# Performance work log

Hardware: AMD Instinct MI355X
Metric: run time of the kernel (lower is better)

## Reference

```python
import jax, jax.numpy as jnp
import numpy as np

B, S, E, H = 8, 2048, 512, 4
D = E // H


def setup_inputs() -> dict:
    key = jax.random.key(0)
    ks = jax.random.split(key, 9)
    std = 0.05  # keras 'normal' initializer default stddev
    return {
        "x": jax.random.normal(ks[0], (B, S, E), dtype=jnp.float32),
        "Wq": jax.random.normal(ks[1], (E, E), dtype=jnp.float32) * std,
        "Wk": jax.random.normal(ks[2], (E, E), dtype=jnp.float32) * std,
        "Wv": jax.random.normal(ks[3], (E, E), dtype=jnp.float32) * std,
        "Wepi": jax.random.normal(ks[4], (S, S), dtype=jnp.float32) * std,
        "bq": jax.random.normal(ks[5], (S, 1), dtype=jnp.float32) * std,
        "bk": jax.random.normal(ks[6], (S, 1), dtype=jnp.float32) * std,
        "bv": jax.random.normal(ks[7], (S, 1), dtype=jnp.float32) * std,
        "bo": jax.random.normal(ks[8], (S, 1), dtype=jnp.float32) * std,
    }


def reference(x, Wq, Wk, Wv, Wepi, bq, bk, bv, bo):
    b, s, e = x.shape
    # QKV projections; [S,1] biases broadcast across the feature dim
    q = x @ Wq + bq  # [B,S,E]
    k = x @ Wk + bk
    v = x @ Wv + bv
    # split heads -> [B,H,S,D]
    q = q.reshape(b, s, H, D).transpose(0, 2, 1, 3)
    k = k.reshape(b, s, H, D).transpose(0, 2, 1, 3)
    v = v.reshape(b, s, H, D).transpose(0, 2, 1, 3)
    # NOTE: source scales by sqrt(seq_length), not sqrt(head_dim)
    scale = 1.0 / np.sqrt(float(s)).astype(np.float32)
    scores = jnp.einsum("bhsd,bhtd->bhst", q, k) * scale  # [B,H,S,S]
    attn = jax.nn.softmax(scores, axis=-1)
    # epigenomic multiplicative mask applied AFTER softmax (broadcast [S,S])
    attn = attn * Wepi
    effect = jnp.einsum("bhst,bhtd->bhsd", attn, v)  # [B,H,S,D]
    effect = effect.transpose(0, 2, 1, 3).reshape(b, s, e) + bo
    # original returns attention in merged-batch layout [B*H, S, S]
    return effect, attn.reshape(b * H, s, s)
```

## Files before the change

### kernel.cpp

```cpp
#include <hip/hip_runtime.h>
#include <hip/hip_bf16.h>

constexpr int Bn = 8, Sn = 2048, En = 512, Hn = 4, Dn = 128;
constexpr int BHn = Bn * Hn;
constexpr int Mqkv = Bn * Sn;

typedef __attribute__((ext_vector_type(8))) short short8;
typedef __attribute__((ext_vector_type(4))) float f32x4;

__device__ __forceinline__ unsigned short f2bf(float f) {
  unsigned int u = __builtin_bit_cast(unsigned int, f);
  u += 0x7FFF + ((u >> 16) & 1);
  return (unsigned short)(u >> 16);
}

__device__ __forceinline__ void bar_pub() {
  asm volatile("s_waitcnt lgkmcnt(0)" ::: "memory");
  __builtin_amdgcn_s_barrier();
  asm volatile("" ::: "memory");
}

__global__ __launch_bounds__(256) void qkv_kernel(
    const float* __restrict__ x, const float* __restrict__ Wq,
    const float* __restrict__ Wk, const float* __restrict__ Wv,
    const float* __restrict__ bq, const float* __restrict__ bk,
    const float* __restrict__ bv, unsigned short* __restrict__ qkv) {
  const int z = blockIdx.z;
  const float* W = (z == 0) ? Wq : (z == 1 ? Wk : Wv);
  const float* bias = (z == 0) ? bq : (z == 1 ? bk : bv);
  unsigned short* out = qkv + (size_t)z * BHn * Sn * Dn;

  __shared__ unsigned short As[128][40];
  __shared__ unsigned short BsT[128][40];

  const int t = threadIdx.x;
  const int l = t & 63, w = t >> 6;
  const int wm = w >> 1, wn = w & 1;
  const int m0 = blockIdx.x * 128, n0 = blockIdx.y * 128;

  f32x4 acc[4][4] = {};

  for (int k0 = 0; k0 < En; k0 += 32) {
    __syncthreads();
#pragma unroll
    for (int i = 0; i < 4; ++i) {
      int idx = t + i * 256;
      int row = idx >> 3, c4 = (idx & 7) * 4;
      float4 v = *reinterpret_cast<const float4*>(&x[(size_t)(m0 + row) * En + k0 + c4]);
      ushort4 p;
      p.x = f2bf(v.x); p.y = f2bf(v.y); p.z = f2bf(v.z); p.w = f2bf(v.w);
      *reinterpret_cast<ushort4*>(&As[row][c4]) = p;
    }
#pragma unroll
    for (int i = 0; i < 4; ++i) {
      int idx = t + i * 256;
      int kk = idx >> 5, c4 = (idx & 31) * 4;
      float4 v = *reinterpret_cast<const float4*>(&W[(size_t)(k0 + kk) * En + n0 + c4]);
      BsT[c4 + 0][kk] = f2bf(v.x);
      BsT[c4 + 1][kk] = f2bf(v.y);
      BsT[c4 + 2][kk] = f2bf(v.z);
      BsT[c4 + 3][kk] = f2bf(v.w);
    }
    __syncthreads();

    const int koff = (l >> 4) * 8;
    short8 a[4], bfr[4];
#pragma unroll
    for (int m = 0; m < 4; ++m)
      a[m] = *reinterpret_cast<const short8*>(&As[wm * 64 + m * 16 + (l & 15)][koff]);
#pragma unroll
    for (int n = 0; n < 4; ++n)
      bfr[n] = *reinterpret_cast<const short8*>(&BsT[wn * 64 + n * 16 + (l & 15)][koff]);
#pragma unroll
    for (int m = 0; m < 4; ++m)
#pragma unroll
      for (int n = 0; n < 4; ++n)
        acc[m][n] = __builtin_amdgcn_mfma_f32_16x16x32_bf16(a[m], bfr[n], acc[m][n], 0, 0, 0);
  }

#pragma unroll
  for (int m = 0; m < 4; ++m)
#pragma unroll
    for (int n = 0; n < 4; ++n)
#pragma unroll
      for (int j = 0; j < 4; ++j) {
        int row = m0 + wm * 64 + m * 16 + (l >> 4) * 4 + j;
        int col = n0 + wn * 64 + n * 16 + (l & 15);
        int s = row & (Sn - 1);
        float v = acc[m][n][j] + bias[s];
        int b = row >> 11;
        int h = col >> 7, d = col & 127;
        out[(size_t)((b * Hn + h) * Sn + s) * Dn + d] = f2bf(v);
      }
}

__global__ __launch_bounds__(256) void vtrans_kernel(
    const unsigned short* __restrict__ v, unsigned short* __restrict__ vT) {
  const int s0 = blockIdx.x * 64, d0 = blockIdx.y * 64;
  const int bh = blockIdx.z;
  const unsigned short* vp = v + (size_t)bh * Sn * Dn;
  unsigned short* op = vT + (size_t)bh * Dn * Sn;
  __shared__ unsigned short Ls[64][72];
  const int t = threadIdx.x;
#pragma unroll
  for (int it = 0; it < 2; ++it) {
    int flat = t + it * 256;
    int r = flat >> 3, cc = flat & 7;
    *reinterpret_cast<short8*>(&Ls[r][cc * 8]) =
        *reinterpret_cast<const short8*>(&vp[(size_t)(s0 + r) * Dn + d0 + cc * 8]);
  }
  __syncthreads();
#pragma unroll
  for (int it = 0; it < 2; ++it) {
    int flat = t + it * 256;
    int d = flat >> 3, sc = flat & 7;
    short8 o;
#pragma unroll
    for (int jo = 0; jo < 8; ++jo) {
      int jj = (jo + sc) & 7;
      o[jj] = (short)Ls[sc * 8 + jj][d];
    }
    *reinterpret_cast<short8*>(&op[(size_t)(d0 + d) * Sn + s0 + sc * 8]) = o;
  }
}

__global__ __launch_bounds__(256, 2) void fused_attn5_kernel(
    const unsigned short* __restrict__ qkv, const unsigned short* __restrict__ vT,
    const float* __restrict__ Wepi, const float* __restrict__ bo,
    float* __restrict__ attn, float* __restrict__ effect) {
  const int bh = blockIdx.y;
  const int s0 = blockIdx.x * 64;
  const unsigned short* qp = qkv + (size_t)bh * Sn * Dn;
  const unsigned short* kp = qkv + (size_t)(BHn + bh) * Sn * Dn;
  const unsigned short* vt = vT + (size_t)bh * Dn * Sn;

  __shared__ unsigned short Kb[2][64 * 128];
  __shared__ unsigned short Vt[2][128 * 64];
  __shared__ unsigned short Ps[2][64 * 64];

  const int t = threadIdx.x, l = t & 63, w = t >> 6;
  const int g = l >> 4, i = l & 15;
  const float scale = 0.022097086912079608f;

  short8 aq[4][4];
#pragma unroll
  for (int sf = 0; sf < 4; ++sf)
#pragma unroll
    for (int ks = 0; ks < 4; ++ks)
      aq[sf][ks] = *reinterpret_cast<const short8*>(
          &qp[(size_t)(s0 + sf * 16 + i) * Dn + ks * 32 + g * 8]);

  int ksrc[4], kdst[4], vsrc[4], vdst[4];
#pragma unroll
  for (int it = 0; it < 4; ++it) {
    int flat = t + it * 256;
    int r = flat >> 4, cc = flat & 15;
    ksrc[it] = r * Dn + cc * 8;
    kdst[it] = r * 128 + ((cc ^ (r & 15)) << 3);
    int d = flat >> 3, ct = flat & 7;
    vsrc[it] = d * Sn + ct * 8;
    vdst[it] = d * 64 + ((ct ^ (d & 7)) << 3);
  }

  short8 kreg[4];
#pragma unroll
  for (int it = 0; it < 4; ++it)
    kreg[it] = *reinterpret_cast<const short8*>(&kp[ksrc[it]]);
#pragma unroll
  for (int it = 0; it < 4; ++it)
    *reinterpret_cast<short8*>(&Kb[0][kdst[it]]) = kreg[it];
#pragma unroll
  for (int it = 0; it < 4; ++it)
    kreg[it] = *reinterpret_cast<const short8*>(&kp[(size_t)64 * Dn + ksrc[it]]);
  bar_pub();

  float rs[4] = {0.f, 0.f, 0.f, 0.f};
  for (int kt = 0; kt < 32; ++kt) {
    const int b = kt & 1;
    f32x4 accT[4] = {};
    __builtin_amdgcn_s_setprio(1);
#pragma unroll
    for (int ks = 0; ks < 4; ++ks) {
      short8 ak = *reinterpret_cast<const short8*>(
          &Kb[b][(w * 16 + i) * 128 + (((ks * 4 + g) ^ i) << 3)]);
#pragma unroll
      for (int sf = 0; sf < 4; ++sf)
        accT[sf] = __builtin_amdgcn_mfma_f32_16x16x32_bf16(ak, aq[sf][ks], accT[sf], 0, 0, 0);
    }
    __builtin_amdgcn_s_setprio(0);
#pragma unroll
    for (int sf = 0; sf < 4; ++sf)
      rs[sf] += __expf(accT[sf][0] * scale) + __expf(accT[sf][1] * scale) +
                __expf(accT[sf][2] * scale) + __expf(accT[sf][3] * scale);
    if (kt < 31) {
#pragma unroll
      for (int it = 0; it < 4; ++it)
        *reinterpret_cast<short8*>(&Kb[b ^ 1][kdst[it]]) = kreg[it];
      if (kt < 30)
#pragma unroll
        for (int it = 0; it < 4; ++it)
          kreg[it] = *reinterpret_cast<const short8*>(
              &kp[(size_t)(kt + 2) * 64 * Dn + ksrc[it]]);
    }
    bar_pub();
  }

  float* wpart = reinterpret_cast<float*>(&Ps[0][0]);
#pragma unroll
  for (int sf = 0; sf < 4; ++sf) {
    float v = rs[sf];
    v += __shfl_xor(v, 16);
    v += __shfl_xor(v, 32);
    if (l < 16) wpart[w * 64 + sf * 16 + l] = v;
  }
  bar_pub();
  float rinv[4];
#pragma unroll
  for (int sf = 0; sf < 4; ++sf) {
    const int s = sf * 16 + i;
    rinv[sf] = 1.0f / (wpart[s] + wpart[64 + s] + wpart[128 + s] + wpart[192 + s]);
  }

  short8 vreg[4];
#pragma unroll
  for (int it = 0; it < 4; ++it)
    kreg[it] = *reinterpret_cast<const short8*>(&kp[ksrc[it]]);
#pragma unroll
  for (int it = 0; it < 4; ++it)
    *reinterpret_cast<short8*>(&Kb[0][kdst[it]]) = kreg[it];
#pragma unroll
  for (int it = 0; it < 4; ++it) {
    kreg[it] = *reinterpret_cast<const short8*>(&kp[(size_t)64 * Dn + ksrc[it]]);
    vreg[it] = *reinterpret_cast<const short8*>(&vt[vsrc[it]]);
  }
  const float* wbase = Wepi + (size_t)(s0 + i) * Sn + w * 16 + g * 4;
  float* abase = attn + (size_t)bh * Sn * Sn + (size_t)(s0 + i) * Sn + w * 16 + g * 4;
  float4 wr[4];
#pragma unroll
  for (int sf = 0; sf < 4; ++sf)
    wr[sf] = *reinterpret_cast<const float4*>(&wbase[(size_t)sf * 16 * Sn]);
  bar_pub();

  f32x4 pv[4][2] = {};
  for (int kt = 0; kt < 32; ++kt) {
    const int b = kt & 1;
    const int t0 = kt * 64;
    f32x4 accT[4] = {};
    __builtin_amdgcn_s_setprio(1);
#pragma unroll
    for (int ks = 0; ks < 4; ++ks) {
      short8 ak = *reinterpret_cast<const short8*>(
          &Kb[b][(w * 16 + i) * 128 + (((ks * 4 + g) ^ i) << 3)]);
#pragma unroll
      for (int sf = 0; sf < 4; ++sf)
        accT[sf] = __builtin_amdgcn_mfma_f32_16x16x32_bf16(ak, aq[sf][ks], accT[sf], 0, 0, 0);
    }
    if (kt > 0) {
#pragma unroll
      for (int ks2 = 0; ks2 < 2; ++ks2) {
        short8 pa[4];
#pragma unroll
        for (int sf = 0; sf < 4; ++sf)
          pa[sf] = *reinterpret_cast<const short8*>(
              &Ps[b ^ 1][(sf * 16 + i) * 64 + (((ks2 * 4 + g) ^ (i & 7)) << 3)]);
#pragma unroll
        for (int nf = 0; nf < 2; ++nf) {
          const int d = w * 32 + nf * 16 + i;
          short8 bv = *reinterpret_cast<const short8*>(
              &Vt[b ^ 1][d * 64 + (((ks2 * 4 + g) ^ (i & 7)) << 3)]);
#pragma unroll
          for (int sf = 0; sf < 4; ++sf)
            pv[sf][nf] =
                __builtin_amdgcn_mfma_f32_16x16x32_bf16(pa[sf], bv, pv[sf][nf], 0, 0, 0);
        }
      }
    }
    __builtin_amdgcn_s_setprio(0);

#pragma unroll
    for (int sf = 0; sf < 4; ++sf) {
      float q0 = __expf(accT[sf][0] * scale) * rinv[sf] * wr[sf].x;
      float q1 = __expf(accT[sf][1] * scale) * rinv[sf] * wr[sf].y;
      float q2 = __expf(accT[sf][2] * scale) * rinv[sf] * wr[sf].z;
      float q3 = __expf(accT[sf][3] * scale) * rinv[sf] * wr[sf].w;
      float4 pf4 = {q0, q1, q2, q3};
      *reinterpret_cast<float4*>(&abase[(size_t)sf * 16 * Sn + t0]) = pf4;
      ushort4 pk;
      pk.x = f2bf(q0); pk.y = f2bf(q1); pk.z = f2bf(q2); pk.w = f2bf(q3);
      const int row = sf * 16 + i;
      *reinterpret_cast<ushort4*>(
          &Ps[b][row * 64 + (((w * 2 + (g >> 1)) ^ (i & 7)) << 3) + (g & 1) * 4]) = pk;
    }
    if (kt < 31)
#pragma unroll
      for (int sf = 0; sf < 4; ++sf)
        wr[sf] = *reinterpret_cast<const float4*>(&wbase[(size_t)sf * 16 * Sn + t0 + 64]);

    if (kt < 31)
#pragma unroll
      for (int it = 0; it < 4; ++it)
        *reinterpret_cast<short8*>(&Kb[b ^ 1][kdst[it]]) = kreg[it];
#pragma unroll
    for (int it = 0; it < 4; ++it)
      *reinterpret_cast<short8*>(&Vt[b][vdst[it]]) = vreg[it];
    if (kt < 30)
#pragma unroll
      for (int it = 0; it < 4; ++it)
        kreg[it] = *reinterpret_cast<const short8*>(
            &kp[(size_t)(kt + 2) * 64 * Dn + ksrc[it]]);
    if (kt < 31)
#pragma unroll
      for (int it = 0; it < 4; ++it)
        vreg[it] = *reinterpret_cast<const short8*>(&vt[t0 + 64 + vsrc[it]]);
    bar_pub();
  }

  __builtin_amdgcn_s_setprio(1);
#pragma unroll
  for (int ks2 = 0; ks2 < 2; ++ks2) {
    short8 pa[4];
#pragma unroll
    for (int sf = 0; sf < 4; ++sf)
      pa[sf] = *reinterpret_cast<const short8*>(
          &Ps[1][(sf * 16 + i) * 64 + (((ks2 * 4 + g) ^ (i & 7)) << 3)]);
#pragma unroll
    for (int nf = 0; nf < 2; ++nf) {
      const int d = w * 32 + nf * 16 + i;
      short8 bv = *reinterpret_cast<const short8*>(
          &Vt[1][d * 64 + (((ks2 * 4 + g) ^ (i & 7)) << 3)]);
#pragma unroll
      for (int sf = 0; sf < 4; ++sf)
        pv[sf][nf] = __builtin_amdgcn_mfma_f32_16x16x32_bf16(pa[sf], bv, pv[sf][nf], 0, 0, 0);
    }
  }
  __builtin_amdgcn_s_setprio(0);

  const int b_ = bh >> 2, h_ = bh & 3;
#pragma unroll
  for (int sf = 0; sf < 4; ++sf)
#pragma unroll
    for (int j = 0; j < 4; ++j) {
      const int row = s0 + sf * 16 + g * 4 + j;
      const float bias = bo[row];
#pragma unroll
      for (int nf = 0; nf < 2; ++nf)
        effect[(size_t)(b_ * Sn + row) * En + h_ * Dn + w * 32 + nf * 16 + i] =
            pv[sf][nf][j] + bias;
    }
}

extern "C" void kernel_launch(void* const* d_in, const int* in_sizes, int n_in,
                              void* d_out, int out_size, void* d_ws, size_t ws_size,
                              hipStream_t stream) {
  const float* x    = (const float*)d_in[0];
  const float* Wq   = (const float*)d_in[1];
  const float* Wk   = (const float*)d_in[2];
  const float* Wv   = (const float*)d_in[3];
  const float* Wepi = (const float*)d_in[4];
  const float* bq   = (const float*)d_in[5];
  const float* bk   = (const float*)d_in[6];
  const float* bv   = (const float*)d_in[7];
  const float* bo   = (const float*)d_in[8];

  float* effect = (float*)d_out;
  float* attn = effect + (size_t)Bn * Sn * En;
  unsigned short* qkv = (unsigned short*)d_ws;
  unsigned short* vT = qkv + (size_t)3 * BHn * Sn * Dn;

  qkv_kernel<<<dim3(Mqkv / 128, En / 128, 3), 256, 0, stream>>>(x, Wq, Wk, Wv, bq, bk, bv, qkv);
  vtrans_kernel<<<dim3(Sn / 64, Dn / 64, BHn), 256, 0, stream>>>(
      qkv + (size_t)2 * BHn * Sn * Dn, vT);
  fused_attn5_kernel<<<dim3(Sn / 64, BHn), 256, 0, stream>>>(qkv, vT, Wepi, bo, attn, effect);
}
```

Before: 406.5 us.

## Restructure fused attention into 32-key tiles with 2x2 warp split for higher occupancy

```diff
diff --git a/kernel.cpp b/kernel.cpp
--- a/kernel.cpp
+++ b/kernel.cpp
@@ -124,7 +124,7 @@
   }
 }
 
-__global__ __launch_bounds__(256, 2) void fused_attn5_kernel(
+__global__ __launch_bounds__(256, 4) void fused_attn6_kernel(
     const unsigned short* __restrict__ qkv, const unsigned short* __restrict__ vT,
     const float* __restrict__ Wepi, const float* __restrict__ bo,
     float* __restrict__ attn, float* __restrict__ effect) {
@@ -134,218 +134,187 @@
   const unsigned short* kp = qkv + (size_t)(BHn + bh) * Sn * Dn;
   const unsigned short* vt = vT + (size_t)bh * Dn * Sn;
 
-  __shared__ unsigned short Kb[2][64 * 128];
-  __shared__ unsigned short Vt[2][128 * 64];
-  __shared__ unsigned short Ps[2][64 * 64];
+  __shared__ unsigned short Kb[2][32 * 128];
+  __shared__ unsigned short Ps[2][64 * 40];
+  __shared__ float red[4][2][16];
 
   const int t = threadIdx.x, l = t & 63, w = t >> 6;
   const int g = l >> 4, i = l & 15;
+  const int th = w & 1;
+  const int sh = w >> 1;
   const float scale = 0.022097086912079608f;
 
-  short8 aq[4][4];
-#pragma unroll
-  for (int sf = 0; sf < 4; ++sf)
+  short8 aq[2][4];
+#pragma unroll
+  for (int sf = 0; sf < 2; ++sf)
 #pragma unroll
     for (int ks = 0; ks < 4; ++ks)
       aq[sf][ks] = *reinterpret_cast<const short8*>(
-          &qp[(size_t)(s0 + sf * 16 + i) * Dn + ks * 32 + g * 8]);
-
-  int ksrc[4], kdst[4], vsrc[4], vdst[4];
-#pragma unroll
-  for (int it = 0; it < 4; ++it) {
+          &qp[(size_t)(s0 + sh * 32 + sf * 16 + i) * Dn + ks * 32 + g * 8]);
+
+  int ksrc[2], kdst[2];
+#pragma unroll
+  for (int it = 0; it < 2; ++it) {
     int flat = t + it * 256;
     int r = flat >> 4, cc = flat & 15;
     ksrc[it] = r * Dn + cc * 8;
     kdst[it] = r * 128 + ((cc ^ (r & 15)) << 3);
-    int d = flat >> 3, ct = flat & 7;
-    vsrc[it] = d * Sn + ct * 8;
-    vdst[it] = d * 64 + ((ct ^ (d & 7)) << 3);
-  }
-
-  short8 kreg[4];
-#pragma unroll
-  for (int it = 0; it < 4; ++it)
+  }
+
+  short8 kreg[2];
+#pragma unroll
+  for (int it = 0; it < 2; ++it)
     kreg[it] = *reinterpret_cast<const short8*>(&kp[ksrc[it]]);
 #pragma unroll
-  for (int it = 0; it < 4; ++it)
+  for (int it = 0; it < 2; ++it)
     *reinterpret_cast<short8*>(&Kb[0][kdst[it]]) = kreg[it];
 #pragma unroll
-  for (int it = 0; it < 4; ++it)
-    kreg[it] = *reinterpret_cast<const short8*>(&kp[(size_t)64 * Dn + ksrc[it]]);
+  for (int it = 0; it < 2; ++it)
+    kreg[it] = *reinterpret_cast<const short8*>(&kp[(size_t)32 * Dn + ksrc[it]]);
   bar_pub();
 
-  float rs[4] = {0.f, 0.f, 0.f, 0.f};
-  for (int kt = 0; kt < 32; ++kt) {
+  float rs[2] = {0.f, 0.f};
+  for (int kt = 0; kt < 64; ++kt) {
     const int b = kt & 1;
-    f32x4 accT[4] = {};
+    f32x4 accT[2] = {};
     __builtin_amdgcn_s_setprio(1);
 #pragma unroll
     for (int ks = 0; ks < 4; ++ks) {
       short8 ak = *reinterpret_cast<const short8*>(
-          &Kb[b][(w * 16 + i) * 128 + (((ks * 4 + g) ^ i) << 3)]);
-#pragma unroll
-      for (int sf = 0; sf < 4; ++sf)
+          &Kb[b][(th * 16 + i) * 128 + (((ks * 4 + g) ^ i) << 3)]);
+#pragma unroll
+      for (int sf = 0; sf < 2; ++sf)
         accT[sf] = __builtin_amdgcn_mfma_f32_16x16x32_bf16(ak, aq[sf][ks], accT[sf], 0, 0, 0);
     }
     __builtin_amdgcn_s_setprio(0);
 #pragma unroll
-    for (int sf = 0; sf < 4; ++sf)
+    for (int sf = 0; sf < 2; ++sf)
       rs[sf] += __expf(accT[sf][0] * scale) + __expf(accT[sf][1] * scale) +
                 __expf(accT[sf][2] * scale) + __expf(accT[sf][3] * scale);
-    if (kt < 31) {
-#pragma unroll
-      for (int it = 0; it < 4; ++it)
+    if (kt < 63) {
+#pragma unroll
+      for (int it = 0; it < 2; ++it)
         *reinterpret_cast<short8*>(&Kb[b ^ 1][kdst[it]]) = kreg[it];
-      if (kt < 30)
-#pragma unroll
-        for (int it = 0; it < 4; ++it)
+      if (kt < 62)
+#pragma unroll
+        for (int it = 0; it < 2; ++it)
           kreg[it] = *reinterpret_cast<const short8*>(
-              &kp[(size_t)(kt + 2) * 64 * Dn + ksrc[it]]);
+              &kp[(size_t)(kt + 2) * 32 * Dn + ksrc[it]]);
     }
     bar_pub();
   }
 
-  float* wpart = reinterpret_cast<float*>(&Ps[0][0]);
-#pragma unroll
-  for (int sf = 0; sf < 4; ++sf) {
+#pragma unroll
+  for (int sf = 0; sf < 2; ++sf) {
     float v = rs[sf];
     v += __shfl_xor(v, 16);
     v += __shfl_xor(v, 32);
-    if (l < 16) wpart[w * 64 + sf * 16 + l] = v;
+    if (l < 16) red[w][sf][l] = v;
   }
   bar_pub();
-  float rinv[4];
-#pragma unroll
-  for (int sf = 0; sf < 4; ++sf) {
-    const int s = sf * 16 + i;
-    rinv[sf] = 1.0f / (wpart[s] + wpart[64 + s] + wpart[128 + s] + wpart[192 + s]);
-  }
-
-  short8 vreg[4];
-#pragma unroll
-  for (int it = 0; it < 4; ++it)
+  float rinv[2];
+#pragma unroll
+  for (int sf = 0; sf < 2; ++sf)
+    rinv[sf] = 1.0f / (red[w][sf][i] + red[w ^ 1][sf][i]);
+
+#pragma unroll
+  for (int it = 0; it < 2; ++it)
     kreg[it] = *reinterpret_cast<const short8*>(&kp[ksrc[it]]);
 #pragma unroll
-  for (int it = 0; it < 4; ++it)
+  for (int it = 0; it < 2; ++it)
     *reinterpret_cast<short8*>(&Kb[0][kdst[it]]) = kreg[it];
 #pragma unroll
-  for (int it = 0; it < 4; ++it) {
-    kreg[it] = *reinterpret_cast<const short8*>(&kp[(size_t)64 * Dn + ksrc[it]]);
-    vreg[it] = *reinterpret_cast<const short8*>(&vt[vsrc[it]]);
-  }
-  const float* wbase = Wepi + (size_t)(s0 + i) * Sn + w * 16 + g * 4;
-  float* abase = attn + (size_t)bh * Sn * Sn + (size_t)(s0 + i) * Sn + w * 16 + g * 4;
-  float4 wr[4];
-#pragma unroll
-  for (int sf = 0; sf < 4; ++sf)
-    wr[sf] = *reinterpret_cast<const float4*>(&wbase[(size_t)sf * 16 * Sn]);
+  for (int it = 0; it < 2; ++it)
+    kreg[it] = *reinterpret_cast<const short8*>(&kp[(size_t)32 * Dn + ksrc[it]]);
   bar_pub();
 
+  const float* wrow = Wepi + (size_t)(s0 + sh * 32 + i) * Sn + th * 16 + g * 4;
+  float* arow = attn + (size_t)bh * Sn * Sn + (size_t)(s0 + sh * 32 + i) * Sn + th * 16 + g * 4;
+
   f32x4 pv[4][2] = {};
-  for (int kt = 0; kt < 32; ++kt) {
+  short8 vreg[2];
+
+  for (int kt = 0; kt < 64; ++kt) {
     const int b = kt & 1;
-    const int t0 = kt * 64;
-    f32x4 accT[4] = {};
+    const int t0 = kt * 32;
+    f32x4 accT[2] = {};
     __builtin_amdgcn_s_setprio(1);
 #pragma unroll
     for (int ks = 0; ks < 4; ++ks) {
       short8 ak = *reinterpret_cast<const short8*>(
-          &Kb[b][(w * 16 + i) * 128 + (((ks * 4 + g) ^ i) << 3)]);
-#pragma unroll
-      for (int sf = 0; sf < 4; ++sf)
+          &Kb[b][(th * 16 + i) * 128 + (((ks * 4 + g) ^ i) << 3)]);
+#pragma unroll
+      for (int sf = 0; sf < 2; ++sf)
         accT[sf] = __builtin_amdgcn_mfma_f32_16x16x32_bf16(ak, aq[sf][ks], accT[sf], 0, 0, 0);
     }
     if (kt > 0) {
 #pragma unroll
-      for (int ks2 = 0; ks2 < 2; ++ks2) {
-        short8 pa[4];
-#pragma unroll
-        for (int sf = 0; sf < 4; ++sf)
-          pa[sf] = *reinterpret_cast<const short8*>(
-              &Ps[b ^ 1][(sf * 16 + i) * 64 + (((ks2 * 4 + g) ^ (i & 7)) << 3)]);
-#pragma unroll
-        for (int nf = 0; nf < 2; ++nf) {
-          const int d = w * 32 + nf * 16 + i;
-          short8 bv = *reinterpret_cast<const short8*>(
-              &Vt[b ^ 1][d * 64 + (((ks2 * 4 + g) ^ (i & 7)) << 3)]);
-#pragma unroll
-          for (int sf = 0; sf < 4; ++sf)
-            pv[sf][nf] =
-                __builtin_amdgcn_mfma_f32_16x16x32_bf16(pa[sf], bv, pv[sf][nf], 0, 0, 0);
-        }
+      for (int pf = 0; pf < 4; ++pf) {
+        short8 pa = *reinterpret_cast<const short8*>(&Ps[b ^ 1][(pf * 16 + i) * 40 + g * 8]);
+#pragma unroll
+        for (int nf = 0; nf < 2; ++nf)
+          pv[pf][nf] = __builtin_amdgcn_mfma_f32_16x16x32_bf16(pa, vreg[nf], pv[pf][nf], 0, 0, 0);
       }
     }
     __builtin_amdgcn_s_setprio(0);
 
 #pragma unroll
-    for (int sf = 0; sf < 4; ++sf) {
-      float q0 = __expf(accT[sf][0] * scale) * rinv[sf] * wr[sf].x;
-      float q1 = __expf(accT[sf][1] * scale) * rinv[sf] * wr[sf].y;
-      float q2 = __expf(accT[sf][2] * scale) * rinv[sf] * wr[sf].z;
-      float q3 = __expf(accT[sf][3] * scale) * rinv[sf] * wr[sf].w;
+    for (int nf = 0; nf < 2; ++nf)
+      vreg[nf] = *reinterpret_cast<const short8*>(
+          &vt[(size_t)(w * 32 + nf * 16 + i) * Sn + t0 + g * 8]);
+
+    float4 w4[2];
+#pragma unroll
+    for (int sf = 0; sf < 2; ++sf)
+      w4[sf] = *reinterpret_cast<const float4*>(&wrow[(size_t)sf * 16 * Sn + t0]);
+#pragma unroll
+    for (int sf = 0; sf < 2; ++sf) {
+      float q0 = __expf(accT[sf][0] * scale) * rinv[sf] * w4[sf].x;
+      float q1 = __expf(accT[sf][1] * scale) * rinv[sf] * w4[sf].y;
+      float q2 = __expf(accT[sf][2] * scale) * rinv[sf] * w4[sf].z;
+      float q3 = __expf(accT[sf][3] * scale) * rinv[sf] * w4[sf].w;
       float4 pf4 = {q0, q1, q2, q3};
-      *reinterpret_cast<float4*>(&abase[(size_t)sf * 16 * Sn + t0]) = pf4;
+      *reinterpret_cast<float4*>(&arow[(size_t)sf * 16 * Sn + t0]) = pf4;
       ushort4 pk;
       pk.x = f2bf(q0); pk.y = f2bf(q1); pk.z = f2bf(q2); pk.w = f2bf(q3);
-      const int row = sf * 16 + i;
       *reinterpret_cast<ushort4*>(
-          &Ps[b][row * 64 + (((w * 2 + (g >> 1)) ^ (i & 7)) << 3) + (g & 1) * 4]) = pk;
-    }
-    if (kt < 31)
-#pragma unroll
-      for (int sf = 0; sf < 4; ++sf)
-        wr[sf] = *reinterpret_cast<const float4*>(&wbase[(size_t)sf * 16 * Sn + t0 + 64]);
-
-    if (kt < 31)
-#pragma unroll
-      for (int it = 0; it < 4; ++it)
+          &Ps[b][(sh * 32 + sf * 16 + i) * 40 + th * 16 + g * 4]) = pk;
+    }
+
+    if (kt < 63) {
+#pragma unroll
+      for (int it = 0; it < 2; ++it)
         *reinterpret_cast<short8*>(&Kb[b ^ 1][kdst[it]]) = kreg[it];
-#pragma unroll
-    for (int it = 0; it < 4; ++it)
-      *reinterpret_cast<short8*>(&Vt[b][vdst[it]]) = vreg[it];
-    if (kt < 30)
-#pragma unroll
-      for (int it = 0; it < 4; ++it)
-        kreg[it] = *reinterpret_cast<const short8*>(
-            &kp[(size_t)(kt + 2) * 64 * Dn + ksrc[it]]);
-    if (kt < 31)
-#pragma unroll
-      for (int it = 0; it < 4; ++it)
-        vreg[it] = *reinterpret_cast<const short8*>(&vt[t0 + 64 + vsrc[it]]);
+      if (kt < 62)
+#pragma unroll
+        for (int it = 0; it < 2; ++it)
+          kreg[it] = *reinterpret_cast<const short8*>(
+              &kp[(size_t)(kt + 2) * 32 * Dn + ksrc[it]]);
+    }
     bar_pub();
   }
 
   __builtin_amdgcn_s_setprio(1);
 #pragma unroll
-  for (int ks2 = 0; ks2 < 2; ++ks2) {
-    short8 pa[4];
-#pragma unroll
-    for (int sf = 0; sf < 4; ++sf)
-      pa[sf] = *reinterpret_cast<const short8*>(
-          &Ps[1][(sf * 16 + i) * 64 + (((ks2 * 4 + g) ^ (i & 7)) << 3)]);
-#pragma unroll
-    for (int nf = 0; nf < 2; ++nf) {
-      const int d = w * 32 + nf * 16 + i;
-      short8 bv = *reinterpret_cast<const short8*>(
-          &Vt[1][d * 64 + (((ks2 * 4 + g) ^ (i & 7)) << 3)]);
-#pragma unroll
-      for (int sf = 0; sf < 4; ++sf)
-        pv[sf][nf] = __builtin_amdgcn_mfma_f32_16x16x32_bf16(pa[sf], bv, pv[sf][nf], 0, 0, 0);
-    }
+  for (int pf = 0; pf < 4; ++pf) {
+    short8 pa = *reinterpret_cast<const short8*>(&Ps[1][(pf * 16 + i) * 40 + g * 8]);
+#pragma unroll
+    for (int nf = 0; nf < 2; ++nf)
+      pv[pf][nf] = __builtin_amdgcn_mfma_f32_16x16x32_bf16(pa, vreg[nf], pv[pf][nf], 0, 0, 0);
   }
   __builtin_amdgcn_s_setprio(0);
 
   const int b_ = bh >> 2, h_ = bh & 3;
 #pragma unroll
-  for (int sf = 0; sf < 4; ++sf)
+  for (int pf = 0; pf < 4; ++pf)
 #pragma unroll
     for (int j = 0; j < 4; ++j) {
-      const int row = s0 + sf * 16 + g * 4 + j;
+      const int row = s0 + pf * 16 + g * 4 + j;
       const float bias = bo[row];
 #pragma unroll
       for (int nf = 0; nf < 2; ++nf)
         effect[(size_t)(b_ * Sn + row) * En + h_ * Dn + w * 32 + nf * 16 + i] =
-            pv[sf][nf][j] + bias;
+            pv[pf][nf][j] + bias;
     }
 }
 
@@ -370,5 +339,5 @@
   qkv_kernel<<<dim3(Mqkv / 128, En / 128, 3), 256, 0, stream>>>(x, Wq, Wk, Wv, bq, bk, bv, qkv);
   vtrans_kernel<<<dim3(Sn / 64, Dn / 64, BHn), 256, 0, stream>>>(
       qkv + (size_t)2 * BHn * Sn * Dn, vT);
-  fused_attn5_kernel<<<dim3(Sn / 64, BHn), 256, 0, stream>>>(qkv, vT, Wepi, bo, attn, effect);
-}
+  fused_attn6_kernel<<<dim3(Sn / 64, BHn), 256, 0, stream>>>(qkv, vT, Wepi, bo, attn, effect);
+}
```

After: 480.4 us. 1.18x slower.
